# Optimization experiments

Measured on AMD Instinct MI355X. Metric: run time of the kernel, lower is better.

Reference implementation:

```python
import jax, jax.numpy as jnp
import numpy as np
from jax import lax

B, D_DATA, D_LAT = 1024, 16384, 256
N_GRID = 256  # silhouette integration grid
EPS = 1e-12


def pairwise_dist(z):
    # z: [n, d] -> Euclidean distance matrix [n, n]
    sq = jnp.sum(z * z, axis=-1)
    d2 = sq[:, None] + sq[None, :] - 2.0 * (z @ z.T)
    return jnp.sqrt(jnp.clip(d2, 0.0) + EPS)


def mst_deaths(dist):
    # H0 persistence of Vietoris-Rips from a distance matrix: births are 0,
    # deaths are the MST edge weights (single-linkage merge heights).
    # Prim's algorithm, vectorized per step, scanned n-1 times.
    n = dist.shape[0]
    in_tree = jnp.zeros((n,), dtype=bool).at[0].set(True)
    mindist = dist[0]

    def step(carry, _):
        in_tree, mindist = carry
        cand = jnp.where(in_tree, jnp.inf, mindist)
        j = jnp.argmin(cand)
        w = cand[j]
        in_tree = in_tree.at[j].set(True)
        mindist = jnp.minimum(mindist, dist[j])
        return (in_tree, mindist), w

    _, deaths = lax.scan(step, (in_tree, mindist), None, length=n - 1)
    return deaths  # [n-1] persistences (births = 0)


def silhouette_value(deaths):
    # Power-1 persistence silhouette phi(t) = sum_j w_j L_j(t) / sum_j w_j,
    # L_j(t) = max(0, min(t - b_j, d_j - t)) with b_j = 0; scalar = mean over grid.
    w = deaths  # persistence^1 weights
    tmax = lax.stop_gradient(jnp.max(deaths))
    t = jnp.linspace(0.0, 1.0, N_GRID) * tmax  # [T]
    tent = jnp.maximum(0.0, jnp.minimum(t[None, :], deaths[:, None] - t[None, :]))
    phi = (w[:, None] * tent).sum(0) / (w.sum() + EPS)
    return jnp.mean(phi)


def setup_inputs() -> dict:
    key = jax.random.key(0)
    k1, k2, k3, k4, k5 = jax.random.split(key, 5)
    return {
        "recon_x": jax.random.normal(k1, (B, D_DATA), dtype=jnp.float32),
        "x": jax.random.normal(k2, (B, D_DATA), dtype=jnp.float32),
        "mu": jax.random.normal(k3, (B, D_LAT), dtype=jnp.float32),
        "logvar": jax.random.normal(k4, (B, D_LAT), dtype=jnp.float32),
        "representations": jax.random.normal(k5, (B, D_LAT), dtype=jnp.float32),
    }


def reference(recon_x, x, mu, logvar, representations):
    recon_weight, kl_weight, topo_weight = 1.0, 0.1, 0.5
    reg_weight = 1.0  # TopologicalRegularization(weight=1.0)

    recon_loss = jnp.mean((recon_x - x) ** 2)
    kl_loss = -0.5 * jnp.mean(1.0 + logvar - mu * mu - jnp.exp(logvar))

    dist = pairwise_dist(representations)
    deaths = mst_deaths(dist)          # dim-0 diagram persistences
    topo_loss = reg_weight * silhouette_value(deaths)

    total = recon_weight * recon_loss + kl_weight * kl_loss + topo_weight * topo_loss
    return total, recon_loss, kl_loss, topo_loss
```

## Files before the change

kernel.cpp:

```cpp
#include <hip/hip_runtime.h>
#include <hip/hip_bf16.h>
#include <math.h>


#define NBLK 1024
#define PBLK 64
#define DBLK 256

__device__ __forceinline__ float sub2(const float4 a, const float4 b) {
  const float dx = a.x - b.x, dy = a.y - b.y, dz = a.z - b.z, dw = a.w - b.w;
  return dx * dx + dy * dy + dz * dz + dw * dw;
}

__global__ __launch_bounds__(256) void init_kernel(unsigned long long* __restrict__ cminb) {
  const int t = threadIdx.x;
  for (int v = t; v < 2048; v += 256) cminb[v] = ~0ull;
}

__global__ __launch_bounds__(256) void prep_kernel(const float* __restrict__ z,
                                                   float* __restrict__ dist,
                                                   unsigned long long* __restrict__ cmin0,
                                                   const float4* __restrict__ rx,
                                                   const float4* __restrict__ x,
                                                   const float4* __restrict__ mu,
                                                   const float4* __restrict__ lv,
                                                   float* __restrict__ partials) {
  __shared__ float A[64][68];
  __shared__ float Bs[64][68];
  __shared__ float sqA[64];
  __shared__ float sqB[64];
  __shared__ float red[8];
  const int t = threadIdx.x;
  const int b = blockIdx.x;

  if (b >= DBLK) {
    const int lb = b - DBLK;
    const int base = lb * 4096 + t;
    float rs0 = 0.f, rs1 = 0.f, rs2 = 0.f, rs3 = 0.f;
#pragma unroll
    for (int kk = 0; kk < 4; ++kk) {
      const int i0 = base + kk * 1024;
      const float4 a0 = rx[i0],       c0 = x[i0];
      const float4 a1 = rx[i0 + 256], c1 = x[i0 + 256];
      const float4 a2 = rx[i0 + 512], c2 = x[i0 + 512];
      const float4 a3 = rx[i0 + 768], c3 = x[i0 + 768];
      rs0 += sub2(a0, c0);
      rs1 += sub2(a1, c1);
      rs2 += sub2(a2, c2);
      rs3 += sub2(a3, c3);
    }
    float rs = (rs0 + rs1) + (rs2 + rs3);
    float ks = 0.f;
    if (lb < 256) {
      const int gid = lb * 256 + t;
      const float4 m = mu[gid], l = lv[gid];
      ks += 1.f + l.x - m.x * m.x - __expf(l.x);
      ks += 1.f + l.y - m.y * m.y - __expf(l.y);
      ks += 1.f + l.z - m.z * m.z - __expf(l.z);
      ks += 1.f + l.w - m.w * m.w - __expf(l.w);
    }
#pragma unroll
    for (int off = 32; off; off >>= 1) {
      rs += __shfl_xor(rs, off);
      ks += __shfl_xor(ks, off);
    }
    if ((t & 63) == 0) { red[t >> 6] = rs; red[4 + (t >> 6)] = ks; }
    __syncthreads();
    if (t == 0) {
      partials[lb] = red[0] + red[1] + red[2] + red[3];
      partials[NBLK + lb] = red[4] + red[5] + red[6] + red[7];
    }
    return;
  }

  const int i0 = (b >> 4) * 64, j0 = (b & 15) * 64;
  const int tx = t & 15;
  const int ty = t >> 4;
  float acc[4][4] = {};
  float psA = 0.f, psB = 0.f;
  const int sr = t >> 2, sc = (t & 3) * 16;
  for (int k0 = 0; k0 < 256; k0 += 64) {
    __syncthreads();
#pragma unroll
    for (int it = 0; it < 4; ++it) {
      int lin = it * 256 + t;
      int row = lin >> 4, q = lin & 15;
      *(float4*)&A[row][q * 4]  = *(const float4*)(z + (i0 + row) * 256 + k0 + q * 4);
      *(float4*)&Bs[row][q * 4] = *(const float4*)(z + (j0 + row) * 256 + k0 + q * 4);
    }
    __syncthreads();
#pragma unroll
    for (int e = 0; e < 16; ++e) {
      const float va = A[sr][sc + e];  psA += va * va;
      const float vb = Bs[sr][sc + e]; psB += vb * vb;
    }
#pragma unroll 4
    for (int k = 0; k < 64; k += 4) {
      float4 av[4], bv[4];
#pragma unroll
      for (int rr = 0; rr < 4; ++rr) av[rr] = *(const float4*)&A[ty + 16 * rr][k];
#pragma unroll
      for (int cc = 0; cc < 4; ++cc) bv[cc] = *(const float4*)&Bs[tx + 16 * cc][k];
#pragma unroll
      for (int rr = 0; rr < 4; ++rr)
#pragma unroll
        for (int cc = 0; cc < 4; ++cc) {
          acc[rr][cc] += av[rr].x * bv[cc].x;
          acc[rr][cc] += av[rr].y * bv[cc].y;
          acc[rr][cc] += av[rr].z * bv[cc].z;
          acc[rr][cc] += av[rr].w * bv[cc].w;
        }
    }
  }
  {
    float s = psA + __shfl_xor(psA, 1); s += __shfl_xor(s, 2);
    if ((t & 3) == 0) sqA[t >> 2] = s;
    float u = psB + __shfl_xor(psB, 1); u += __shfl_xor(u, 2);
    if ((t & 3) == 0) sqB[t >> 2] = u;
  }
  __syncthreads();
  unsigned long long rowbest[4] = {~0ull, ~0ull, ~0ull, ~0ull};
#pragma unroll
  for (int rr = 0; rr < 4; ++rr) {
    const int i = i0 + ty + 16 * rr;
    const float sqi = sqA[ty + 16 * rr];
#pragma unroll
    for (int cc = 0; cc < 4; ++cc) {
      const int j = j0 + tx + 16 * cc;
      const float d2 = sqi + sqB[tx + 16 * cc] - 2.f * acc[rr][cc];
      const float d = sqrtf(fmaxf(d2, 0.f) + 1e-12f);
      dist[i * 1024 + j] = (j == i) ? 0.f : d;
      if (j != i) {
        const int lo = i < j ? i : j;
        const int hi = i + j - lo;
        const unsigned long long key =
            ((unsigned long long)__float_as_uint(d) << 32)
          | (unsigned long long)((lo << 10) | hi);
        if (key < rowbest[rr]) rowbest[rr] = key;
      }
    }
  }
#pragma unroll
  for (int rr = 0; rr < 4; ++rr) {
    unsigned long long best = rowbest[rr];
#pragma unroll
    for (int off = 8; off; off >>= 1) {
      const unsigned int blo = __shfl_xor((unsigned int)best, off);
      const unsigned int bhi = __shfl_xor((unsigned int)(best >> 32), off);
      const unsigned long long o = ((unsigned long long)bhi << 32) | blo;
      if (o < best) best = o;
    }
    if (tx == 0) {
      unsigned long long* p = &cmin0[i0 + ty + 16 * rr];
      const unsigned long long cur =
          __hip_atomic_load(p, __ATOMIC_RELAXED, __HIP_MEMORY_SCOPE_AGENT);
      if (best < cur) atomicMin(p, best);
    }
  }
}

__device__ __forceinline__ int phase_b_dev(const unsigned long long* __restrict__ cbuf,
                                           int* scomp, unsigned long long* cl,
                                           int* pnew, int* sred,
                                           bool record, float* sdeaths, int* scnt) {
  const int t = threadIdx.x;
  for (int v = t; v < 1024; v += 256)
    cl[v] = __hip_atomic_load(&cbuf[v], __ATOMIC_RELAXED, __HIP_MEMORY_SCOPE_AGENT);
  if (t == 0) sred[0] = 0;
  __syncthreads();
  for (int v = t; v < 1024; v += 256) {
    int parent = scomp[v];
    if (parent == v) {
      const unsigned long long key = cl[v];
      if (key != ~0ull) {
        const int lo = (int)((key >> 10) & 1023), hi = (int)(key & 1023);
        const int clo = scomp[lo], chi = scomp[hi];
        const int other = (clo == v) ? chi : clo;
        const bool mutual = (cl[other] == key);
        if (record && (!mutual || v < other)) {
          const int pos = atomicAdd(scnt, 1);
          sdeaths[pos] = __uint_as_float((unsigned int)(key >> 32));
        }
        parent = (mutual && v < other) ? v : other;
      }
    }
    pnew[v] = parent;
  }
  __syncthreads();
#pragma unroll
  for (int it = 0; it < 2; ++it) {
    int q0 = pnew[pnew[t]];
    int q1 = pnew[pnew[t + 256]];
    int q2 = pnew[pnew[t + 512]];
    int q3 = pnew[pnew[t + 768]];
    __syncthreads();
    pnew[t] = q0; pnew[t + 256] = q1; pnew[t + 512] = q2; pnew[t + 768] = q3;
    __syncthreads();
  }
  int nroots = 0;
#pragma unroll
  for (int q = 0; q < 4; ++q) {
    const int v = t + q * 256;
    int p = pnew[v];
    while (p != pnew[p]) p = pnew[p];
    scomp[v] = p;
    if (p == v) ++nroots;
  }
  atomicAdd(&sred[0], nroots);
  __syncthreads();
  return sred[0];
}

__global__ __launch_bounds__(256) void mst_kernel(float* __restrict__ dist,
                                                  unsigned long long* __restrict__ cminb,
                                                  const float* __restrict__ partials,
                                                  float* __restrict__ out) {
  __shared__ int scomp[1024];
  __shared__ int pnew[1024];
  __shared__ unsigned long long cl[1024];
  __shared__ float sdeaths[1023];
  __shared__ int sred[2];
  __shared__ float redf[12];
  const int t = threadIdx.x;
  const int b = blockIdx.x;
  const bool rec = (b == 0);
  int* slots = (int*)dist;

  for (int v = t; v < 1024; v += 256) scomp[v] = v;
  if (t == 0) sred[1] = 0;
  if (t < 16)
    __hip_atomic_store(&cminb[2048 + b * 16 + t], ~0ull,
                       __ATOMIC_RELAXED, __HIP_MEMORY_SCOPE_AGENT);
  __syncthreads();

  int ncomp = phase_b_dev(cminb, scomp, cl, pnew, sred, rec, sdeaths, &sred[1]);

  const int lane = t & 63;
  const int w = t >> 6;
  for (int r = 1; r < 10 && ncomp > 1; ++r) {
    unsigned long long* cbuf = cminb + (r % 3) * 1024;
#pragma unroll
    for (int q = 0; q < 4; ++q) {
      const int i = b * 16 + w * 4 + q;
      const int ci = scomp[i];
      const float* row = dist + i * 1024;
      unsigned long long best = ~0ull;
#pragma unroll
      for (int k = 0; k < 4; ++k) {
        const int j0 = lane * 4 + k * 256;
        const float4 d4 = *(const float4*)(row + j0);
        const int4 c4 = *(const int4*)(&scomp[j0]);
        const float dv[4] = {d4.x, d4.y, d4.z, d4.w};
        const int cv[4] = {c4.x, c4.y, c4.z, c4.w};
#pragma unroll
        for (int c = 0; c < 4; ++c) {
          if (cv[c] != ci) {
            const int j = j0 + c;
            const int lo = i < j ? i : j;
            const int hi = i + j - lo;
            const unsigned long long key =
                ((unsigned long long)__float_as_uint(dv[c]) << 32)
              | (unsigned long long)((lo << 10) | hi);
            if (key < best) best = key;
          }
        }
      }
#pragma unroll
      for (int off = 32; off; off >>= 1) {
        const unsigned int blo = __shfl_xor((unsigned int)best, off);
        const unsigned int bhi = __shfl_xor((unsigned int)(best >> 32), off);
        const unsigned long long o = ((unsigned long long)bhi << 32) | blo;
        if (o < best) best = o;
      }
      if (lane == 0 && best != ~0ull) {
        const unsigned long long cur =
            __hip_atomic_load(&cbuf[ci], __ATOMIC_RELAXED, __HIP_MEMORY_SCOPE_AGENT);
        if (best < cur) atomicMin(&cbuf[ci], best);
      }
    }
    __syncthreads();
    if (t == 0)
      __hip_atomic_store(&slots[(size_t)(16 * b + 1) * 1025], r,
                         __ATOMIC_RELEASE, __HIP_MEMORY_SCOPE_AGENT);
    if (t < 64) {
      const size_t sidx = (size_t)(16 * t + 1) * 1025;
      for (;;) {
        const int v = __hip_atomic_load(&slots[sidx], __ATOMIC_ACQUIRE,
                                        __HIP_MEMORY_SCOPE_AGENT);
        if (__all(v >= r)) break;
        __builtin_amdgcn_s_sleep(1);
      }
    }
    __syncthreads();
    if (t < 16)
      __hip_atomic_store(&cminb[((r - 1) % 3) * 1024 + b * 16 + t], ~0ull,
                         __ATOMIC_RELAXED, __HIP_MEMORY_SCOPE_AGENT);
    ncomp = phase_b_dev(cbuf, scomp, cl, pnew, sred, rec, sdeaths, &sred[1]);
  }

  if (b != 0) return;
  float lmax = 0.f, lsum = 0.f;
  for (int v = t; v < 1023; v += 256) {
    const float d = sdeaths[v];
    lmax = fmaxf(lmax, d);
    lsum += d;
  }
#pragma unroll
  for (int off = 32; off; off >>= 1) {
    lmax = fmaxf(lmax, __shfl_xor(lmax, off));
    lsum += __shfl_xor(lsum, off);
  }
  if ((t & 63) == 0) { redf[t >> 6] = lmax; redf[4 + (t >> 6)] = lsum; }
  __syncthreads();
  const float tmax = fmaxf(fmaxf(redf[0], redf[1]), fmaxf(redf[2], redf[3]));
  const float wsum = redf[4] + redf[5] + redf[6] + redf[7];
  const float tt = (float)t * (1.0f / 255.0f) * tmax;
  float acc = 0.f;
  for (int j = 0; j < 1023; ++j) {
    const float dj = sdeaths[j];
    acc += dj * fmaxf(fminf(tt, dj - tt), 0.f);
  }
  float phi = acc / (wsum + 1e-12f);
  float rs = 0.f, ks = 0.f;
  for (int v = t; v < 1024; v += 256) { rs += partials[v]; ks += partials[1024 + v]; }
#pragma unroll
  for (int off = 32; off; off >>= 1) {
    phi += __shfl_xor(phi, off);
    rs += __shfl_xor(rs, off);
    ks += __shfl_xor(ks, off);
  }
  __syncthreads();
  if ((t & 63) == 0) { redf[t >> 6] = phi; redf[4 + (t >> 6)] = rs; redf[8 + (t >> 6)] = ks; }
  __syncthreads();
  if (t == 0) {
    const float topo = (redf[0] + redf[1] + redf[2] + redf[3]) * (1.f / 256.f);
    const float recon = (redf[4] + redf[5] + redf[6] + redf[7]) * (1.f / 16777216.f);
    const float kl = -0.5f * (redf[8] + redf[9] + redf[10] + redf[11]) * (1.f / 262144.f);
    const float total = recon + 0.1f * kl + 0.5f * topo;
    out[0] = (float)__float2bfloat16(total);
    out[1] = (float)__float2bfloat16(recon);
    out[2] = (float)__float2bfloat16(kl);
    out[3] = (float)__float2bfloat16(topo);
  }
}

extern "C" void kernel_launch(void* const* d_in, const int* in_sizes, int n_in,
                              void* d_out, int out_size, void* d_ws, size_t ws_size,
                              hipStream_t stream) {
  const float* rx = (const float*)d_in[0];
  const float* x  = (const float*)d_in[1];
  const float* mu = (const float*)d_in[2];
  const float* lv = (const float*)d_in[3];
  const float* z  = (const float*)d_in[4];

  float* wsf = (float*)d_ws;
  unsigned long long* cminb = (unsigned long long*)wsf;
  float* partials = wsf + 6144;
  float* dist     = wsf + 8192;
  float* out      = (float*)d_out;

  init_kernel<<<1, 256, 0, stream>>>(cminb);
  prep_kernel<<<NBLK + DBLK, 256, 0, stream>>>(z, dist, cminb,
                                               (const float4*)rx, (const float4*)x,
                                               (const float4*)mu, (const float4*)lv,
                                               partials);
  mst_kernel<<<PBLK, 256, 0, stream>>>(dist, cminb, partials, out);
}
```

Measured before the change: 205.1 us.

## Finish MST with a contracted-graph Prim once component count is small

```diff
diff --git a/kernel.cpp b/kernel.cpp
--- a/kernel.cpp
+++ b/kernel.cpp
@@ -6,6 +6,7 @@
 #define NBLK 1024
 #define PBLK 64
 #define DBLK 256
+#define CMAX 45
 
 __device__ __forceinline__ float sub2(const float4 a, const float4 b) {
   const float dx = a.x - b.x, dy = a.y - b.y, dz = a.z - b.z, dw = a.w - b.w;
@@ -218,6 +219,7 @@
   __shared__ int scomp[1024];
   __shared__ int pnew[1024];
   __shared__ unsigned long long cl[1024];
+  __shared__ unsigned int cmat[CMAX * CMAX];
   __shared__ float sdeaths[1023];
   __shared__ int sred[2];
   __shared__ float redf[12];
@@ -237,7 +239,8 @@
 
   const int lane = t & 63;
   const int w = t >> 6;
-  for (int r = 1; r < 10 && ncomp > 1; ++r) {
+  int r = 1;
+  for (; r < 10 && ncomp > CMAX; ++r) {
     unsigned long long* cbuf = cminb + (r % 3) * 1024;
 #pragma unroll
     for (int q = 0; q < 4; ++q) {
@@ -297,6 +300,111 @@
                          __ATOMIC_RELAXED, __HIP_MEMORY_SCOPE_AGENT);
     ncomp = phase_b_dev(cbuf, scomp, cl, pnew, sred, rec, sdeaths, &sred[1]);
   }
+  const int r_exit = r;
+
+  if (ncomp > 1) {
+    const int c = ncomp;
+    int c_t = 0, rmask = 0;
+#pragma unroll
+    for (int q = 0; q < 4; ++q) {
+      const int v = 4 * t + q;
+      const int ir = (scomp[v] == v) ? 1 : 0;
+      rmask |= ir << q;
+      c_t += ir;
+    }
+    int scan = c_t;
+#pragma unroll
+    for (int off = 1; off < 64; off <<= 1) {
+      const int n = __shfl_up(scan, off);
+      if (lane >= off) scan += n;
+    }
+    if (lane == 63) ((int*)redf)[w] = scan;
+    for (int e = t; e < c * c; e += 256) cmat[e] = ~0u;
+    __syncthreads();
+    int woff = 0;
+    for (int u = 0; u < w; ++u) woff += ((int*)redf)[u];
+    int rk = woff + (scan - c_t);
+    int* rankmap = (int*)cl;
+#pragma unroll
+    for (int q = 0; q < 4; ++q) {
+      const int v = 4 * t + q;
+      if (rmask & (1 << q)) { rankmap[v] = rk; ++rk; }
+    }
+    __syncthreads();
+    for (int v = t; v < 1024; v += 256) pnew[v] = rankmap[scomp[v]];
+    __syncthreads();
+#pragma unroll
+    for (int q = 0; q < 4; ++q) {
+      const int i = b * 16 + w * 4 + q;
+      const int a = pnew[i];
+      const float* row = dist + i * 1024;
+#pragma unroll
+      for (int k = 0; k < 4; ++k) {
+        const int j0 = lane * 4 + k * 256;
+        const float4 d4 = *(const float4*)(row + j0);
+        const int4 c4 = *(const int4*)(&pnew[j0]);
+        const float dv[4] = {d4.x, d4.y, d4.z, d4.w};
+        const int cv[4] = {c4.x, c4.y, c4.z, c4.w};
+#pragma unroll
+        for (int cc = 0; cc < 4; ++cc) {
+          if (cv[cc] != a) atomicMin(&cmat[a * c + cv[cc]], __float_as_uint(dv[cc]));
+        }
+      }
+    }
+    __syncthreads();
+    unsigned int* gcm = (unsigned int*)(cminb + (r_exit % 3) * 1024);
+    for (int e = t; e < c * c; e += 256) {
+      const unsigned int u = cmat[e];
+      if (u != ~0u) atomicMin(&gcm[e], u);
+    }
+    __threadfence();
+    __syncthreads();
+    if (t == 0)
+      __hip_atomic_store(&slots[(size_t)(16 * b + 1) * 1025], r_exit,
+                         __ATOMIC_RELEASE, __HIP_MEMORY_SCOPE_AGENT);
+    if (b != 0) return;
+    if (t < 64) {
+      const size_t sidx = (size_t)(16 * t + 1) * 1025;
+      for (;;) {
+        const int v = __hip_atomic_load(&slots[sidx], __ATOMIC_ACQUIRE,
+                                        __HIP_MEMORY_SCOPE_AGENT);
+        if (__all(v >= r_exit)) break;
+        __builtin_amdgcn_s_sleep(1);
+      }
+    }
+    __syncthreads();
+    for (int e = t; e < c * c; e += 256)
+      cmat[e] = __hip_atomic_load(&gcm[e], __ATOMIC_RELAXED, __HIP_MEMORY_SCOPE_AGENT);
+    __syncthreads();
+    const int base = sred[1];
+    if (t < 64) {
+      const int e = lane;
+      bool intree = (e == 0) || (e >= c);
+      unsigned int md = (e > 0 && e < c) ? cmat[e] : ~0u;
+      for (int step = 0; step < c - 1; ++step) {
+        unsigned long long key =
+            intree ? ~0ull : (((unsigned long long)md << 32) | (unsigned int)e);
+#pragma unroll
+        for (int off = 32; off; off >>= 1) {
+          const unsigned int blo = __shfl_xor((unsigned int)key, off);
+          const unsigned int bhi = __shfl_xor((unsigned int)(key >> 32), off);
+          const unsigned long long o = ((unsigned long long)bhi << 32) | blo;
+          if (o < key) key = o;
+        }
+        const unsigned int wb = (unsigned int)(key >> 32);
+        const int bc = (int)(key & 0xffffffffu);
+        if (lane == 0) sdeaths[base + step] = __uint_as_float(wb);
+        if (e == bc) { intree = true; md = ~0u; }
+        else if (!intree) {
+          const unsigned int nv = cmat[bc * c + e];
+          if (nv < md) md = nv;
+        }
+      }
+    }
+    __syncthreads();
+  } else if (b != 0) {
+    return;
+  }
 
   if (b != 0) return;
   float lmax = 0.f, lsum = 0.f;
```

Measured after the change: 206.6 us. About the same (+0.7%).
